# Performance work log

Hardware: AMD Instinct MI355X
Metric: run time of the kernel (lower is better)

## Reference

```python
import jax, jax.numpy as jnp
import numpy as np

FEAT = 64
K = 16
K4 = K // 4
EPS = 1e-5  # BatchNorm eps (inference mode with running stats)


def _conv1x1(x, w, b):
    # x: (B, Cin, N, K), w: (Cout, Cin), b: (Cout,)
    return jnp.einsum('oc,bcnk->bonk', w, x) + b[None, :, None, None]


def _bn(x, g, be, m, v):
    # inference-mode BatchNorm2d over channel axis 1
    inv = g / jnp.sqrt(v + EPS)
    return (x - m[None, :, None, None]) * inv[None, :, None, None] + be[None, :, None, None]


def setup_inputs() -> dict:
    key = jax.random.key(0)
    ks = jax.random.split(key, 20)
    B, N, M = 4, 8192, 8192
    d = {}
    d['original_pts'] = jax.random.normal(ks[0], (B, 3, M), dtype=jnp.float32)
    d['query_pts'] = jax.random.normal(ks[1], (B, 3, N), dtype=jnp.float32)
    d['local_feat'] = jax.random.normal(ks[2], (B, FEAT, M), dtype=jnp.float32)
    # mlp_0: Conv2D(3, FEAT) with BN + ReLU
    d['w0'] = jax.random.normal(ks[3], (FEAT, 3), dtype=jnp.float32) * 0.2
    d['b0'] = jax.random.normal(ks[4], (FEAT,), dtype=jnp.float32) * 0.01
    d['g0'] = 1.0 + 0.1 * jax.random.normal(ks[5], (FEAT,), dtype=jnp.float32)
    d['be0'] = 0.01 * jax.random.normal(ks[6], (FEAT,), dtype=jnp.float32)
    d['m0'] = 0.01 * jax.random.normal(ks[7], (FEAT,), dtype=jnp.float32)
    d['v0'] = jax.random.uniform(ks[8], (FEAT,), dtype=jnp.float32, minval=0.5, maxval=1.5)
    # mlp_1: Conv2D(FEAT, FEAT) with BN + ReLU
    d['w1'] = jax.random.normal(ks[9], (FEAT, FEAT), dtype=jnp.float32) * 0.1
    d['b1'] = jax.random.normal(ks[10], (FEAT,), dtype=jnp.float32) * 0.01
    d['g1'] = 1.0 + 0.1 * jax.random.normal(ks[11], (FEAT,), dtype=jnp.float32)
    d['be1'] = 0.01 * jax.random.normal(ks[12], (FEAT,), dtype=jnp.float32)
    d['m1'] = 0.01 * jax.random.normal(ks[13], (FEAT,), dtype=jnp.float32)
    d['v1'] = jax.random.uniform(ks[14], (FEAT,), dtype=jnp.float32, minval=0.5, maxval=1.5)
    # mlp_2: Conv2D(2*FEAT, 1), no BN, no ReLU
    d['w2'] = jax.random.normal(ks[15], (1, 2 * FEAT), dtype=jnp.float32) * 0.1
    d['b2'] = jax.random.normal(ks[16], (1,), dtype=jnp.float32) * 0.01
    return d


def reference(original_pts, query_pts, local_feat,
              w0, b0, g0, be0, m0, v0,
              w1, b1, g1, be1, m1, v1,
              w2, b2):
    B, _, N = query_pts.shape
    # --- KNN: squared distances (B, N, M), take K smallest ---
    q2 = jnp.sum(query_pts ** 2, axis=1)          # (B, N)
    o2 = jnp.sum(original_pts ** 2, axis=1)       # (B, M)
    cross = jnp.einsum('bcn,bcm->bnm', query_pts, original_pts)
    d2 = q2[:, :, None] + o2[:, None, :] - 2.0 * cross
    _, knn_idx = jax.lax.top_k(-d2, K)            # (B, N, K)

    # gather neighbor coords: (B, 3, N, K)
    knn_pts = jax.vmap(lambda pts, idx: pts[:, idx])(original_pts, knn_idx)
    # gather local features for first K//4 neighbors: (B, FEAT, N, K4)
    patch_feat = jax.vmap(lambda f, idx: f[:, idx])(local_feat, knn_idx[:, :, :K4])

    relative_pts = knn_pts - query_pts[:, :, :, None]  # (B, 3, N, K)
    feat0 = jax.nn.relu(_bn(_conv1x1(relative_pts, w0, b0), g0, be0, m0, v0))  # (B, F, N, K)
    feat_g = jnp.max(feat0, axis=3, keepdims=True)                              # (B, F, N, 1)
    relative_feat = jax.nn.relu(_bn(_conv1x1(feat0, w1, b1), g1, be1, m1, v1))[:, :, :, :K4]
    feat2 = jnp.concatenate(
        [relative_feat, jnp.broadcast_to(feat_g, (B, FEAT, N, K4))], axis=1)    # (B, 2F, N, K4)
    weight = jax.nn.sigmoid(_conv1x1(feat2, w2, b2))                            # (B, 1, N, K4)
    query_feat = (1.0 - weight) * relative_feat + weight * patch_feat
    return jnp.sum(query_feat, axis=-1)  # (B, FEAT, N)
```

## Files before the change

kernel.cpp:

```cpp
#include <hip/hip_runtime.h>
#include <cstdint>

#define M_PTS 8192
#define N_QRY 8192
#define BATCH 4

typedef unsigned long long ull;

__device__ __forceinline__ float d2_exact(float qx, float qy, float qz, float q2, float4 p) {
#pragma clang fp contract(off)
  float dot = (qx * p.x + qy * p.y) + qz * p.z;
  return (q2 + p.w) - 2.0f * dot;
}

__device__ __forceinline__ unsigned flipf(float d) {
  unsigned u = __float_as_uint(d);
  return u ^ ((unsigned)((int)u >> 31) | 0x80000000u);
}

__device__ __forceinline__ int lane_prefix(unsigned long long m) {
  return __builtin_amdgcn_mbcnt_hi((unsigned)(m >> 32),
         __builtin_amdgcn_mbcnt_lo((unsigned)m, 0));
}

__device__ __forceinline__ void ld_lds16(const float4* g, float4* l) {
  __builtin_amdgcn_global_load_lds((const __attribute__((address_space(1))) void*)g,
                                   (__attribute__((address_space(3))) void*)l, 16, 0, 0);
}

__device__ __forceinline__ float tau16(float mn) {
  float lo = mn, hi = mn;
#pragma unroll
  for (int j = 1; j < 64; j <<= 1) {
    lo = fminf(lo, __shfl_xor(lo, j));
    hi = fmaxf(hi, __shfl_xor(hi, j));
  }
#pragma unroll
  for (int it = 0; it < 10; it++) {
    float mid = 0.5f * (lo + hi);
    int cnt = __popcll(__ballot(mn <= mid));
    if (cnt >= 16) hi = mid; else lo = mid;
  }
  return hi;
}

__device__ __forceinline__ ull bsort64(ull v, int lane) {
#pragma unroll
  for (int k = 2; k <= 64; k <<= 1) {
#pragma unroll
    for (int j = k >> 1; j >= 1; j >>= 1) {
      ull o = __shfl_xor(v, j);
      bool keepmin = (((lane & k) == 0) == ((lane & j) == 0));
      ull lo = v < o ? v : o;
      ull hi = v < o ? o : v;
      v = keepmin ? lo : hi;
    }
  }
  return v;
}

__global__ void pack_pts(const float* __restrict__ src, float4* __restrict__ dst, int total) {
#pragma clang fp contract(off)
  int i = blockIdx.x * 256 + threadIdx.x;
  if (i >= total) return;
  int b = i >> 13, m = i & (M_PTS - 1);
  const float* s = src + (size_t)b * 3 * M_PTS;
  float x = s[m], y = s[M_PTS + m], z = s[2 * M_PTS + m];
  float ss = (x * x + y * y) + z * z;
  dst[i] = make_float4(x, y, z, ss);
}

__global__ void transpose_lf(const float* __restrict__ lf, float* __restrict__ lfT) {
  __shared__ float tile[64][65];
  int bb = blockIdx.x >> 7;
  int m0 = (blockIdx.x & 127) << 6;
  int tm = threadIdx.x & 63;
  int tc = threadIdx.x >> 6;
  const float* src = lf + (size_t)bb * 64 * M_PTS;
#pragma unroll
  for (int i = 0; i < 16; i++) {
    int ch = i * 4 + tc;
    tile[ch][tm] = src[(size_t)ch * M_PTS + m0 + tm];
  }
  __syncthreads();
  float* dst = lfT + ((size_t)bb * M_PTS + m0) * 64;
#pragma unroll
  for (int i = 0; i < 16; i++) {
    int mm = i * 4 + tc;
    dst[(size_t)mm * 64 + tm] = tile[tm][mm];
  }
}

__global__ void __launch_bounds__(256, 7) knn_kernel(const float4* __restrict__ pp,
                                                     const float4* __restrict__ qp,
                                                     int* __restrict__ knn_out) {
  __shared__ float4 spts[2][512];
  __shared__ ull cbuf[8][96];
  const int tid = threadIdx.x;
  const int lane = tid & 63;
  const int wave = tid >> 6;
  const int b = blockIdx.x >> 10;
  const int qa = blockIdx.x * 8 + wave * 2;
  const float4* pb = pp + ((size_t)b << 13);

  const float4 A4 = qp[qa];
  const float4 B4 = qp[qa + 1];
  const float axA = -2.0f * A4.x, ayA = -2.0f * A4.y, azA = -2.0f * A4.z;
  const float axB = -2.0f * B4.x, ayB = -2.0f * B4.y, azB = -2.0f * B4.z;

  int cntA = 0, cntB = 0;
  unsigned* cqA = (unsigned*)cbuf[wave * 2 + 0];
  unsigned* cqB = (unsigned*)cbuf[wave * 2 + 1];

  float mnA = 3.402823466e38f, mnB = 3.402823466e38f;
  float tauA = 0.0f, tauB = 0.0f;

  auto stage = [&](float4* dst, int s) {
#pragma unroll
    for (int i = 0; i < 2; i++) {
      const float4* g = pb + s * 512 + i * 256 + wave * 64 + lane;
      ld_lds16(g, &dst[i * 256 + wave * 64]);
    }
  };

  auto minpass = [&](const float4* sp) {
#pragma unroll
    for (int j = 0; j < 8; j++) {
      float4 p = sp[j * 64 + lane];
      mnA = fminf(mnA, __builtin_fmaf(axA, p.x, __builtin_fmaf(ayA, p.y,
                       __builtin_fmaf(azA, p.z, p.w))));
      mnB = fminf(mnB, __builtin_fmaf(axB, p.x, __builtin_fmaf(ayB, p.y,
                       __builtin_fmaf(azB, p.z, p.w))));
    }
  };

  auto collect = [&](float e, float tau, unsigned* cq, int& cnt, unsigned idx) {
    bool pred = e <= tau;
    unsigned long long mask = __ballot(pred);
    if (mask) {
      int pos = cnt + lane_prefix(mask);
      if (pred && pos < 192) cq[pos] = idx;
      cnt += __popcll(mask);
    }
  };

  auto fused = [&](const float4* sp, unsigned base) {
#pragma unroll
    for (int j = 0; j < 8; j++) {
      float4 p = sp[j * 64 + lane];
      float ea = __builtin_fmaf(axA, p.x, __builtin_fmaf(ayA, p.y,
                 __builtin_fmaf(azA, p.z, p.w)));
      float eb = __builtin_fmaf(axB, p.x, __builtin_fmaf(ayB, p.y,
                 __builtin_fmaf(azB, p.z, p.w)));
      mnA = fminf(mnA, ea);
      mnB = fminf(mnB, eb);
      unsigned idx = base + j * 64 + lane;
      collect(ea, tauA, cqA, cntA, idx);
      collect(eb, tauB, cqB, cntB, idx);
    }
  };

  stage(spts[0], 0);
  __syncthreads();
  stage(spts[1], 1);
  minpass(spts[0]);
  __syncthreads();
  minpass(spts[1]);
  tauA = tau16(mnA) + 0.01f;
  tauB = tau16(mnB) + 0.01f;
  fused(spts[0], 0);
  fused(spts[1], 512);
  __syncthreads();
  stage(spts[0], 2);
  __syncthreads();

  for (int s = 2; s < 16; ++s) {
    if (s < 15) stage(spts[(s + 1) & 1], s + 1);
    fused(spts[s & 1], (unsigned)(s * 512));
    if (s == 3 || s == 7 || s == 11) {
      tauA = fminf(tauA, tau16(mnA) + 0.01f);
      tauB = fminf(tauB, tau16(mnB) + 0.01f);
    }
    __syncthreads();
  }

  auto finalize = [&](ull* cb, int cnt, int gq,
                      float qx, float qy, float qz, float q2) {
    unsigned* cq = (unsigned*)cb;
    int E = cnt < 192 ? cnt : 192;
    unsigned i0 = (lane < E) ? cq[lane] : 0u;
    unsigned i1 = (lane + 64 < E) ? cq[lane + 64] : 0u;
    unsigned i2 = (lane + 128 < E) ? cq[lane + 128] : 0u;
    float4 p0 = pb[i0];
    float4 p1 = pb[i1];
    float4 p2 = pb[i2];
    ull k0 = ~0ull, k1 = ~0ull, k2 = ~0ull;
    if (lane < E)
      k0 = ((ull)flipf(d2_exact(qx, qy, qz, q2, p0)) << 32) | i0;
    if (lane + 64 < E)
      k1 = ((ull)flipf(d2_exact(qx, qy, qz, q2, p1)) << 32) | i1;
    if (lane + 128 < E)
      k2 = ((ull)flipf(d2_exact(qx, qy, qz, q2, p2)) << 32) | i2;
    ull ml = k0 < k1 ? k0 : k1;
    if (k2 < ml) ml = k2;
    ull T = __shfl(bsort64(ml, lane), 15);
    int c2 = 0;
    {
      bool pr = k0 <= T; ull m = __ballot(pr);
      int pos = c2 + lane_prefix(m);
      if (pr) cb[pos] = k0;
      c2 += __popcll(m);
    }
    {
      bool pr = k1 <= T; ull m = __ballot(pr);
      int pos = c2 + lane_prefix(m);
      if (pr) cb[pos] = k1;
      c2 += __popcll(m);
    }
    {
      bool pr = k2 <= T; ull m = __ballot(pr);
      int pos = c2 + lane_prefix(m);
      if (pr) cb[pos] = k2;
      c2 += __popcll(m);
    }
    ull kk = (lane < c2) ? cb[lane] : ~0ull;
    ull fin = bsort64(kk, lane);
    if (lane < 16) knn_out[(size_t)gq * 16 + lane] = (int)(unsigned)fin;
  };

  finalize(cbuf[wave * 2 + 0], cntA, qa,     A4.x, A4.y, A4.z, A4.w);
  finalize(cbuf[wave * 2 + 1], cntB, qa + 1, B4.x, B4.y, B4.z, B4.w);
}

__global__ void __launch_bounds__(256, 4) feat_kernel(
    const float4* __restrict__ pp, const float4* __restrict__ qp,
    const int* __restrict__ knn, const float* __restrict__ lfT,
    const float* __restrict__ w0, const float* __restrict__ b0,
    const float* __restrict__ g0, const float* __restrict__ be0,
    const float* __restrict__ m0, const float* __restrict__ v0,
    const float* __restrict__ w1, const float* __restrict__ b1,
    const float* __restrict__ g1, const float* __restrict__ be1,
    const float* __restrict__ m1, const float* __restrict__ v1,
    const float* __restrict__ w2, const float* __restrict__ b2,
    float* __restrict__ out) {
  __shared__ float4 relbuf[4][16];
  __shared__ float4 f0v[4][64];
  __shared__ float outbuf[64][17];
  const int tid = threadIdx.x;
  const int lane = tid & 63;
  const int wave = tid >> 6;
  const int gq0 = blockIdx.x * 16;
  const int b = gq0 >> 13;

  const float inv0 = g0[lane] / sqrtf(v0[lane] + 1e-5f);
  const float w00 = w0[lane * 3 + 0] * inv0;
  const float w01 = w0[lane * 3 + 1] * inv0;
  const float w02 = w0[lane * 3 + 2] * inv0;
  const float bb0 = (b0[lane] - m0[lane]) * inv0 + be0[lane];
  const float inv1 = g1[lane] / sqrtf(v1[lane] + 1e-5f);
  const float bb1 = (b1[lane] - m1[lane]) * inv1 + be1[lane];

  float w1s[64];
#pragma unroll
  for (int i = 0; i < 16; i++) {
    float4 t = ((const float4*)(w1 + (size_t)lane * 64))[i];
    w1s[i * 4 + 0] = t.x; w1s[i * 4 + 1] = t.y;
    w1s[i * 4 + 2] = t.z; w1s[i * 4 + 3] = t.w;
  }
#pragma unroll
  for (int k = 0; k < 64; k++) asm volatile("" : "+v"(w1s[k]));

  const float w2a = w2[lane], w2b = w2[64 + lane];
  const float bias2 = b2[0];
  const float4* pb = pp + ((size_t)b << 13);
  const float* lfb = lfT + (((size_t)b << 13)) * 64;

  for (int qi = 0; qi < 4; qi++) {
    const int gq = gq0 + wave * 4 + qi;
    const float4 q4 = qp[gq];
    int nk = knn[(size_t)gq * 16 + (lane & 15)];
    float4 pk = pb[nk];
    if (lane < 16)
      relbuf[wave][lane] = make_float4(pk.x - q4.x, pk.y - q4.y, pk.z - q4.z, 0.0f);

    float g = 0.0f, f0 = 0, f1 = 0, f2 = 0, f3 = 0;
#pragma unroll
    for (int k = 0; k < 16; k++) {
      float4 r = relbuf[wave][k];
      float y = fmaxf(0.0f, w00 * r.x + w01 * r.y + w02 * r.z + bb0);
      g = fmaxf(g, y);
      if (k == 0) f0 = y; else if (k == 1) f1 = y;
      else if (k == 2) f2 = y; else if (k == 3) f3 = y;
    }
    f0v[wave][lane] = make_float4(f0, f1, f2, f3);

    float a0 = 0, a1 = 0, a2 = 0, a3 = 0;
#pragma unroll
    for (int c2 = 0; c2 < 64; c2++) {
      float w = w1s[c2];
      float4 fb = f0v[wave][c2];
      a0 = fmaf(w, fb.x, a0); a1 = fmaf(w, fb.y, a1);
      a2 = fmaf(w, fb.z, a2); a3 = fmaf(w, fb.w, a3);
    }
    float r0 = fmaxf(0.0f, fmaf(a0, inv1, bb1));
    float r1 = fmaxf(0.0f, fmaf(a1, inv1, bb1));
    float r2 = fmaxf(0.0f, fmaf(a2, inv1, bb1));
    float r3 = fmaxf(0.0f, fmaf(a3, inv1, bb1));

    int i0 = __shfl(nk, 0), i1 = __shfl(nk, 1), i2 = __shfl(nk, 2), i3 = __shfl(nk, 3);
    float p0 = lfb[(size_t)i0 * 64 + lane];
    float p1 = lfb[(size_t)i1 * 64 + lane];
    float p2 = lfb[(size_t)i2 * 64 + lane];
    float p3 = lfb[(size_t)i3 * 64 + lane];

    float s0 = w2a * r0, s1 = w2a * r1, s2 = w2a * r2, s3 = w2a * r3, tg = w2b * g;
#pragma unroll
    for (int j = 1; j < 64; j <<= 1) {
      s0 += __shfl_xor(s0, j);
      s1 += __shfl_xor(s1, j);
      s2 += __shfl_xor(s2, j);
      s3 += __shfl_xor(s3, j);
      tg += __shfl_xor(tg, j);
    }
    float wk0 = 1.0f / (1.0f + __expf(-(s0 + tg + bias2)));
    float wk1 = 1.0f / (1.0f + __expf(-(s1 + tg + bias2)));
    float wk2 = 1.0f / (1.0f + __expf(-(s2 + tg + bias2)));
    float wk3 = 1.0f / (1.0f + __expf(-(s3 + tg + bias2)));

    float oc = ((1.0f - wk0) * r0 + wk0 * p0)
             + ((1.0f - wk1) * r1 + wk1 * p1)
             + ((1.0f - wk2) * r2 + wk2 * p2)
             + ((1.0f - wk3) * r3 + wk3 * p3);
    outbuf[lane][wave * 4 + qi] = oc;
  }
  __syncthreads();

  int c = tid >> 2, j = tid & 3;
  float4 o4 = make_float4(outbuf[c][j * 4 + 0], outbuf[c][j * 4 + 1],
                          outbuf[c][j * 4 + 2], outbuf[c][j * 4 + 3]);
  *(float4*)(out + (((size_t)(b * 64 + c)) << 13) + (gq0 & (N_QRY - 1)) + j * 4) = o4;
}

extern "C" void kernel_launch(void* const* d_in, const int* in_sizes, int n_in,
                              void* d_out, int out_size, void* d_ws, size_t ws_size,
                              hipStream_t stream) {
  (void)in_sizes; (void)n_in; (void)out_size; (void)ws_size;
  const float* original_pts = (const float*)d_in[0];
  const float* query_pts   = (const float*)d_in[1];
  const float* local_feat  = (const float*)d_in[2];
  const float* w0 = (const float*)d_in[3];
  const float* b0 = (const float*)d_in[4];
  const float* g0 = (const float*)d_in[5];
  const float* be0 = (const float*)d_in[6];
  const float* m0 = (const float*)d_in[7];
  const float* v0 = (const float*)d_in[8];
  const float* w1 = (const float*)d_in[9];
  const float* b1 = (const float*)d_in[10];
  const float* g1 = (const float*)d_in[11];
  const float* be1 = (const float*)d_in[12];
  const float* m1 = (const float*)d_in[13];
  const float* v1 = (const float*)d_in[14];
  const float* w2 = (const float*)d_in[15];
  const float* b2 = (const float*)d_in[16];
  float* out = (float*)d_out;

  char* ws = (char*)d_ws;
  float4* pp  = (float4*)(ws);
  float4* qp  = (float4*)(ws + 524288);
  float*  lfT = (float*)(ws + 1048576);
  int*    knn = (int*)(ws + 9437184);

  pack_pts<<<128, 256, 0, stream>>>(original_pts, pp, BATCH * M_PTS);
  pack_pts<<<128, 256, 0, stream>>>(query_pts, qp, BATCH * N_QRY);
  transpose_lf<<<512, 256, 0, stream>>>(local_feat, lfT);
  knn_kernel<<<4096, 256, 0, stream>>>(pp, qp, knn);
  feat_kernel<<<2048, 256, 0, stream>>>(pp, qp, knn, lfT,
                                        w0, b0, g0, be0, m0, v0,
                                        w1, b1, g1, be1, m1, v1,
                                        w2, b2, out);
}
```

Baseline: 257.8 us.

## Process four queries per wave in KNN kernel to raise point reuse

Each wave now scans the staged point tiles for four queries instead of two, halving the block count and the number of times each LDS tile is loaded and read per query. The double-buffered loop is unrolled by two so the buffer index is static, and the threshold refresh schedule is slightly altered. The extra per-query registers lower the occupancy bound from 7 to 5 blocks, and the dropped final tau refresh may admit more candidates.

```diff
diff --git a/kernel.cpp b/kernel.cpp
--- a/kernel.cpp
+++ b/kernel.cpp
@@ -91,29 +91,31 @@
   }
 }
 
-__global__ void __launch_bounds__(256, 7) knn_kernel(const float4* __restrict__ pp,
+__global__ void __launch_bounds__(256, 5) knn_kernel(const float4* __restrict__ pp,
                                                      const float4* __restrict__ qp,
                                                      int* __restrict__ knn_out) {
   __shared__ float4 spts[2][512];
-  __shared__ ull cbuf[8][96];
+  __shared__ ull cbuf[16][96];
   const int tid = threadIdx.x;
   const int lane = tid & 63;
   const int wave = tid >> 6;
-  const int b = blockIdx.x >> 10;
-  const int qa = blockIdx.x * 8 + wave * 2;
+  const int b = blockIdx.x >> 9;
+  const int qa = blockIdx.x * 16 + wave * 4;
   const float4* pb = pp + ((size_t)b << 13);
 
-  const float4 A4 = qp[qa];
-  const float4 B4 = qp[qa + 1];
-  const float axA = -2.0f * A4.x, ayA = -2.0f * A4.y, azA = -2.0f * A4.z;
-  const float axB = -2.0f * B4.x, ayB = -2.0f * B4.y, azB = -2.0f * B4.z;
-
-  int cntA = 0, cntB = 0;
-  unsigned* cqA = (unsigned*)cbuf[wave * 2 + 0];
-  unsigned* cqB = (unsigned*)cbuf[wave * 2 + 1];
-
-  float mnA = 3.402823466e38f, mnB = 3.402823466e38f;
-  float tauA = 0.0f, tauB = 0.0f;
+  float4 Q[4];
+  float ax[4], ay[4], az[4], mn[4], tau[4];
+  int cnt[4];
+  unsigned* cq[4];
+#pragma unroll
+  for (int i = 0; i < 4; i++) {
+    Q[i] = qp[qa + i];
+    ax[i] = -2.0f * Q[i].x; ay[i] = -2.0f * Q[i].y; az[i] = -2.0f * Q[i].z;
+    mn[i] = 3.402823466e38f;
+    tau[i] = 0.0f;
+    cnt[i] = 0;
+    cq[i] = (unsigned*)cbuf[wave * 4 + i];
+  }
 
   auto stage = [&](float4* dst, int s) {
 #pragma unroll
@@ -127,20 +129,10 @@
 #pragma unroll
     for (int j = 0; j < 8; j++) {
       float4 p = sp[j * 64 + lane];
-      mnA = fminf(mnA, __builtin_fmaf(axA, p.x, __builtin_fmaf(ayA, p.y,
-                       __builtin_fmaf(azA, p.z, p.w))));
-      mnB = fminf(mnB, __builtin_fmaf(axB, p.x, __builtin_fmaf(ayB, p.y,
-                       __builtin_fmaf(azB, p.z, p.w))));
-    }
-  };
-
-  auto collect = [&](float e, float tau, unsigned* cq, int& cnt, unsigned idx) {
-    bool pred = e <= tau;
-    unsigned long long mask = __ballot(pred);
-    if (mask) {
-      int pos = cnt + lane_prefix(mask);
-      if (pred && pos < 192) cq[pos] = idx;
-      cnt += __popcll(mask);
+#pragma unroll
+      for (int i = 0; i < 4; i++)
+        mn[i] = fminf(mn[i], __builtin_fmaf(ax[i], p.x, __builtin_fmaf(ay[i], p.y,
+                            __builtin_fmaf(az[i], p.z, p.w))));
     }
   };
 
@@ -148,15 +140,21 @@
 #pragma unroll
     for (int j = 0; j < 8; j++) {
       float4 p = sp[j * 64 + lane];
-      float ea = __builtin_fmaf(axA, p.x, __builtin_fmaf(ayA, p.y,
-                 __builtin_fmaf(azA, p.z, p.w)));
-      float eb = __builtin_fmaf(axB, p.x, __builtin_fmaf(ayB, p.y,
-                 __builtin_fmaf(azB, p.z, p.w)));
-      mnA = fminf(mnA, ea);
-      mnB = fminf(mnB, eb);
+      asm volatile("" : "+v"(p.x), "+v"(p.y), "+v"(p.z), "+v"(p.w));
       unsigned idx = base + j * 64 + lane;
-      collect(ea, tauA, cqA, cntA, idx);
-      collect(eb, tauB, cqB, cntB, idx);
+#pragma unroll
+      for (int i = 0; i < 4; i++) {
+        float e = __builtin_fmaf(ax[i], p.x, __builtin_fmaf(ay[i], p.y,
+                  __builtin_fmaf(az[i], p.z, p.w)));
+        mn[i] = fminf(mn[i], e);
+        bool pred = e <= tau[i];
+        unsigned long long mask = __ballot(pred);
+        if (mask) {
+          int pos = cnt[i] + lane_prefix(mask);
+          if (pred && pos < 192) cq[i][pos] = idx;
+          cnt[i] += __popcll(mask);
+        }
+      }
     }
   };
 
@@ -166,31 +164,36 @@
   minpass(spts[0]);
   __syncthreads();
   minpass(spts[1]);
-  tauA = tau16(mnA) + 0.01f;
-  tauB = tau16(mnB) + 0.01f;
+#pragma unroll
+  for (int i = 0; i < 4; i++)
+    tau[i] = tau16(mn[i]) + 0.01f;
   fused(spts[0], 0);
   fused(spts[1], 512);
   __syncthreads();
   stage(spts[0], 2);
   __syncthreads();
 
-  for (int s = 2; s < 16; ++s) {
-    if (s < 15) stage(spts[(s + 1) & 1], s + 1);
-    fused(spts[s & 1], (unsigned)(s * 512));
-    if (s == 3 || s == 7 || s == 11) {
-      tauA = fminf(tauA, tau16(mnA) + 0.01f);
-      tauB = fminf(tauB, tau16(mnB) + 0.01f);
-    }
+  for (int sb = 2; sb < 16; sb += 2) {
+    if (sb + 1 < 16) stage(spts[1], sb + 1);
+    fused(spts[0], (unsigned)(sb * 512));
     __syncthreads();
-  }
-
-  auto finalize = [&](ull* cb, int cnt, int gq,
+    if (sb + 2 < 16) stage(spts[0], sb + 2);
+    fused(spts[1], (unsigned)((sb + 1) * 512));
+    if (sb == 2 || sb == 6) {
+#pragma unroll
+      for (int i = 0; i < 4; i++)
+        tau[i] = fminf(tau[i], tau16(mn[i]) + 0.01f);
+    }
+    __syncthreads();
+  }
+
+  auto finalize = [&](ull* cb, int cntq, int gq,
                       float qx, float qy, float qz, float q2) {
-    unsigned* cq = (unsigned*)cb;
-    int E = cnt < 192 ? cnt : 192;
-    unsigned i0 = (lane < E) ? cq[lane] : 0u;
-    unsigned i1 = (lane + 64 < E) ? cq[lane + 64] : 0u;
-    unsigned i2 = (lane + 128 < E) ? cq[lane + 128] : 0u;
+    unsigned* cu = (unsigned*)cb;
+    int E = cntq < 192 ? cntq : 192;
+    unsigned i0 = (lane < E) ? cu[lane] : 0u;
+    unsigned i1 = (lane + 64 < E) ? cu[lane + 64] : 0u;
+    unsigned i2 = (lane + 128 < E) ? cu[lane + 128] : 0u;
     float4 p0 = pb[i0];
     float4 p1 = pb[i1];
     float4 p2 = pb[i2];
@@ -228,8 +231,9 @@
     if (lane < 16) knn_out[(size_t)gq * 16 + lane] = (int)(unsigned)fin;
   };
 
-  finalize(cbuf[wave * 2 + 0], cntA, qa,     A4.x, A4.y, A4.z, A4.w);
-  finalize(cbuf[wave * 2 + 1], cntB, qa + 1, B4.x, B4.y, B4.z, B4.w);
+#pragma unroll
+  for (int i = 0; i < 4; i++)
+    finalize(cbuf[wave * 4 + i], cnt[i], qa + i, Q[i].x, Q[i].y, Q[i].z, Q[i].w);
 }
 
 __global__ void __launch_bounds__(256, 4) feat_kernel(
@@ -373,7 +377,7 @@
   pack_pts<<<128, 256, 0, stream>>>(original_pts, pp, BATCH * M_PTS);
   pack_pts<<<128, 256, 0, stream>>>(query_pts, qp, BATCH * N_QRY);
   transpose_lf<<<512, 256, 0, stream>>>(local_feat, lfT);
-  knn_kernel<<<4096, 256, 0, stream>>>(pp, qp, knn);
+  knn_kernel<<<2048, 256, 0, stream>>>(pp, qp, knn);
   feat_kernel<<<2048, 256, 0, stream>>>(pp, qp, knn, lfT,
                                         w0, b0, g0, be0, m0, v0,
                                         w1, b1, g1, be1, m1, v1,
```

Result: slower. 282.0 us (+9.4%).
